# Performance work log

Measured on AMD Instinct MI355X. Metric: run time of the kernel, lower is better.

## Reference

```python
import jax, jax.numpy as jnp
import numpy as np

HIDDEN = 2048
HEADS = 16
HEAD_DIM = HIDDEN // HEADS


def setup_inputs() -> dict:
    key = jax.random.key(0)
    ks = jax.random.split(key, 9)
    s = 0.02
    return {
        "hidden_state": jax.random.normal(ks[0], (2, 2048, HIDDEN), dtype=jnp.float32),
        "Wq": jax.random.normal(ks[1], (HIDDEN, HIDDEN), dtype=jnp.float32) * s,
        "bq": jnp.zeros((HIDDEN,), dtype=jnp.float32),
        "Wk": jax.random.normal(ks[2], (HIDDEN, HIDDEN), dtype=jnp.float32) * s,
        "bk": jnp.zeros((HIDDEN,), dtype=jnp.float32),
        "Wv": jax.random.normal(ks[3], (HIDDEN, HIDDEN), dtype=jnp.float32) * s,
        "bv": jnp.zeros((HIDDEN,), dtype=jnp.float32),
        "Wo": jax.random.normal(ks[4], (HIDDEN, HIDDEN), dtype=jnp.float32) * s,
        "bo": jnp.zeros((HIDDEN,), dtype=jnp.float32),
    }


def _split_head(x):
    b, s, _ = x.shape
    return x.reshape(b, s, HEADS, HEAD_DIM).transpose(0, 2, 1, 3)  # [B,H,S,D]


def reference(hidden_state, Wq, bq, Wk, bk, Wv, bv, Wo, bo):
    scale = 1.0 / (HEAD_DIM ** 0.5)
    # nn.Linear: x @ W.T + b
    q = _split_head(hidden_state @ Wq.T + bq)
    k = _split_head(hidden_state @ Wk.T + bk)
    v = _split_head(hidden_state @ Wv.T + bv)
    scores = jnp.einsum("bhqd,bhkd->bhqk", q, k) * scale  # [B,H,S,S]
    probs = jax.nn.softmax(scores, axis=-1)
    # dropout treated as identity (eval mode)
    out = jnp.einsum("bhqk,bhkd->bhqd", probs, v)  # [B,H,S,D]
    b, h, s, d = out.shape
    out = out.transpose(0, 2, 1, 3).reshape(b, s, h * d)
    return out @ Wo.T + bo
```

## Files before the change

kernel.cpp:

```cpp
#include <hip/hip_runtime.h>
#include <hip/hip_bf16.h>


typedef __attribute__((ext_vector_type(8))) short bf16x8;
typedef __attribute__((ext_vector_type(4))) float f32x4;
typedef unsigned short ushort_t;

#define MFMA_16x16x32(a, b, c) __builtin_amdgcn_mfma_f32_16x16x32_bf16((a), (b), (c), 0, 0, 0)

__device__ __forceinline__ ushort_t f2bf(float f) {
  unsigned int u = __builtin_bit_cast(unsigned int, f);
  u += 0x7fffu + ((u >> 16) & 1u);
  return (ushort_t)(u >> 16);
}

__device__ __forceinline__ void gload_lds16(const void* g, void* lds) {
  __builtin_amdgcn_global_load_lds(
      (const __attribute__((address_space(1))) unsigned int*)g,
      (__attribute__((address_space(3))) unsigned int*)(unsigned int)(unsigned long long)lds,
      16, 0, 0);
}

__global__ __launch_bounds__(256) void f2bf_kernel(const float* __restrict__ in,
                                                   ushort_t* __restrict__ out, int n4) {
  int i = blockIdx.x * blockDim.x + threadIdx.x;
  const int stride = gridDim.x * blockDim.x;
  for (; i < n4; i += stride) {
    const float4 v = ((const float4*)in)[i];
    ushort4 o;
    o.x = f2bf(v.x); o.y = f2bf(v.y); o.z = f2bf(v.z); o.w = f2bf(v.w);
    ((ushort4*)out)[i] = o;
  }
}

template <int SWAPV>
__global__ __launch_bounds__(512) void qkv_gemm(
    const ushort_t* __restrict__ A,
    const ushort_t* __restrict__ W,
    const float* __restrict__ bq, const float* __restrict__ bk,
    const float* __restrict__ bv,
    ushort_t* __restrict__ Qs, ushort_t* __restrict__ Ks,
    ushort_t* __restrict__ Vts, int nbx, int bcol0) {
  constexpr int K = 2048, NT = K / 32;
  extern __shared__ char sm[];
  const int tid = threadIdx.x;
  const int wave = tid >> 6, lane = tid & 63;
  const int g = lane >> 4, l15 = lane & 15;
  const int wr = wave >> 2, wc = wave & 3;

  const int bid = blockIdx.x;
  const int chunk = (nbx * 16) >> 3;
  const int sw = (bid & 7) * chunk + (bid >> 3);
  const int bx = sw % nbx, by = sw / nbx;
  const int brow = by * 256, bcol = bcol0 + bx * 256;

  const ushort_t* srcA[2];
  const ushort_t* srcB[2];
#pragma unroll
  for (int j = 0; j < 2; ++j) {
    const int p = (wave * 2 + j) * 64 + lane;
    const int row = p >> 2;
    const int col = (p & 3) ^ ((row >> 1) & 3);
    srcA[j] = A + (size_t)(brow + row) * K + col * 8;
    srcB[j] = W + (size_t)(bcol + row) * K + col * 8;
  }

  const int fph = (l15 >> 1) & 3;
  const int aOff = (wr * 128 + l15) * 64 + ((g ^ fph) << 4);
  const int bOff = (wc * 64 + l15) * 64 + ((g ^ fph) << 4) + 16384;

  char* p0 = sm;
  char* p1 = sm + 32768;
  char* p2 = sm + 65536;

#define STAGE_A(P, t)                                                        \
  {                                                                          \
    gload_lds16(srcA[0] + (t) * 32, (P) + (wave * 2 + 0) * 1024);            \
    gload_lds16(srcA[1] + (t) * 32, (P) + (wave * 2 + 1) * 1024);            \
  }
#define STAGE_B(P, t)                                                        \
  {                                                                          \
    gload_lds16(srcB[0] + (t) * 32, (P) + 16384 + (wave * 2 + 0) * 1024);    \
    gload_lds16(srcB[1] + (t) * 32, (P) + 16384 + (wave * 2 + 1) * 1024);    \
  }

  const f32x4 fzero = {0.f, 0.f, 0.f, 0.f};
  f32x4 acc[8][4];
#pragma unroll
  for (int i = 0; i < 8; ++i)
#pragma unroll
    for (int j = 0; j < 4; ++j) acc[i][j] = fzero;

  STAGE_A(p0, 0); STAGE_B(p0, 0);
  STAGE_A(p1, 1); STAGE_B(p1, 1);
  asm volatile("s_waitcnt vmcnt(4)" ::: "memory");
  __builtin_amdgcn_sched_barrier(0);
  __builtin_amdgcn_s_barrier();
  __builtin_amdgcn_sched_barrier(0);

  for (int kt = 0; kt < NT; ++kt) {
    const bool doStage = (kt < NT - 2);
    if (doStage) STAGE_A(p2, kt + 2);
    bf16x8 bfr[4], afr[4];
#pragma unroll
    for (int j = 0; j < 4; ++j) bfr[j] = *(const bf16x8*)(p0 + bOff + j * 1024);
#pragma unroll
    for (int i = 0; i < 4; ++i) afr[i] = *(const bf16x8*)(p0 + aOff + i * 1024);
    __builtin_amdgcn_s_setprio(1);
#pragma unroll
    for (int i = 0; i < 4; ++i)
#pragma unroll
      for (int j = 0; j < 4; ++j)
        acc[i][j] = SWAPV ? MFMA_16x16x32(bfr[j], afr[i], acc[i][j])
                          : MFMA_16x16x32(afr[i], bfr[j], acc[i][j]);
    __builtin_amdgcn_s_setprio(0);
    if (doStage) STAGE_B(p2, kt + 2);
#pragma unroll
    for (int i = 0; i < 4; ++i) afr[i] = *(const bf16x8*)(p0 + aOff + (4 + i) * 1024);
    __builtin_amdgcn_s_setprio(1);
#pragma unroll
    for (int i = 0; i < 4; ++i)
#pragma unroll
      for (int j = 0; j < 4; ++j)
        acc[4 + i][j] = SWAPV ? MFMA_16x16x32(bfr[j], afr[i], acc[4 + i][j])
                              : MFMA_16x16x32(afr[i], bfr[j], acc[4 + i][j]);
    __builtin_amdgcn_s_setprio(0);
    if (doStage) {
      asm volatile("s_waitcnt vmcnt(4) lgkmcnt(0)" ::: "memory");
    } else {
      asm volatile("s_waitcnt vmcnt(0) lgkmcnt(0)" ::: "memory");
    }
    __builtin_amdgcn_sched_barrier(0);
    __builtin_amdgcn_s_barrier();
    __builtin_amdgcn_sched_barrier(0);
    char* t = p0; p0 = p1; p1 = p2; p2 = t;
  }
#undef STAGE_A
#undef STAGE_B

  if (!SWAPV) {
    const int seg = bcol >> 11;
    const float* bias = (seg == 0) ? bq : bk;
    ushort_t* out = (seg == 0) ? Qs : Ks;
#pragma unroll
    for (int j = 0; j < 4; ++j) {
      const int n = (bcol + wc * 64 + j * 16 + l15) & 2047;
      const float bb = bias[n];
      const int h = n >> 7, d = n & 127;
#pragma unroll
      for (int i = 0; i < 8; ++i) {
#pragma unroll
        for (int r = 0; r < 4; ++r) {
          const int grow = brow + wr * 128 + i * 16 + g * 4 + r;
          const int b_ = grow >> 11, s_ = grow & 2047;
          out[(((size_t)b_ * 16 + h) * 2048 + s_) * 128 + d] =
              f2bf(acc[i][j][r] + bb);
        }
      }
    }
  } else {
#pragma unroll
    for (int j = 0; j < 4; ++j) {
#pragma unroll
      for (int r = 0; r < 4; ++r) {
        const int n = (bcol + wc * 64 + j * 16 + g * 4 + r) & 2047;
        const float bb = bv[n];
        const int h = n >> 7, d = n & 127;
#pragma unroll
        for (int i = 0; i < 8; ++i) {
          const int m = brow + wr * 128 + i * 16 + l15;
          const int b_ = m >> 11, s_ = m & 2047;
          Vts[(((size_t)b_ * 16 + h) * 128 + d) * 2048 + s_] =
              f2bf(acc[i][j][r] + bb);
        }
      }
    }
  }
}

__global__ __launch_bounds__(256) void gemm_bt_kernel(const ushort_t* __restrict__ A,
                                                      const ushort_t* __restrict__ B,
                                                      const float* __restrict__ bias,
                                                      float* __restrict__ Cout,
                                                      int M, int N, int K) {
  __shared__ __align__(16) char smem[16384];
  char* sA = smem;
  char* sB = smem + 8192;
  const int tid = threadIdx.x;
  const int wave = tid >> 6;
  const int lane = tid & 63;
  const int wr = wave >> 1, wc = wave & 1;
  const int brow = blockIdx.y * 128;
  const int bcol = blockIdx.x * 128;

  const f32x4 fzero = {0.f, 0.f, 0.f, 0.f};
  f32x4 acc[4][4];
#pragma unroll
  for (int i = 0; i < 4; ++i)
#pragma unroll
    for (int j = 0; j < 4; ++j) acc[i][j] = fzero;

  const int srow = lane >> 2;
  const int koff = (lane & 3) * 8;

  for (int kt = 0; kt < K; kt += 32) {
#pragma unroll
    for (int c = 0; c < 2; ++c) {
      const int ch = wave + c * 4;
      gload_lds16(A + (size_t)(brow + ch * 16 + srow) * K + kt + koff, sA + ch * 1024);
      gload_lds16(B + (size_t)(bcol + ch * 16 + srow) * K + kt + koff, sB + ch * 1024);
    }
    __syncthreads();
    bf16x8 af[4], bfr[4];
#pragma unroll
    for (int i = 0; i < 4; ++i)
      af[i] = *(const bf16x8*)(sA + (wr * 64 + i * 16 + (lane & 15)) * 64 + (lane >> 4) * 16);
#pragma unroll
    for (int j = 0; j < 4; ++j)
      bfr[j] = *(const bf16x8*)(sB + (wc * 64 + j * 16 + (lane & 15)) * 64 + (lane >> 4) * 16);
#pragma unroll
    for (int i = 0; i < 4; ++i)
#pragma unroll
      for (int j = 0; j < 4; ++j) acc[i][j] = MFMA_16x16x32(af[i], bfr[j], acc[i][j]);
    __syncthreads();
  }

#pragma unroll
  for (int i = 0; i < 4; ++i)
#pragma unroll
    for (int j = 0; j < 4; ++j)
#pragma unroll
      for (int r = 0; r < 4; ++r) {
        const int row = brow + wr * 64 + i * 16 + (lane >> 4) * 4 + r;
        const int col = bcol + wc * 64 + j * 16 + (lane & 15);
        Cout[(size_t)row * N + col] = acc[i][j][r] + bias[col];
      }
}

__global__ __launch_bounds__(256) void attn_kernel(const ushort_t* __restrict__ Q,
                                                   const ushort_t* __restrict__ K,
                                                   const ushort_t* __restrict__ Vt,
                                                   ushort_t* __restrict__ O) {
  constexpr int S = 2048, D = 128, H = 16;
  __shared__ __align__(16) char smem[16384 + 16384 + 9216];
  char* sK = smem;
  char* sVt = smem + 16384;
  char* sP = smem + 32768;

  const int tid = threadIdx.x;
  const int wave = tid >> 6;
  const int lane = tid & 63;
  const int g = lane >> 4;
  const int l15 = lane & 15;
  const int qt = blockIdx.x & 31;
  const int bh = blockIdx.x >> 5;
  const int b = bh >> 4, h = bh & 15;

  const ushort_t* Qb = Q + (size_t)bh * S * D;
  const char* Kb = (const char*)(K + (size_t)bh * S * D);
  const char* Vtb = (const char*)(Vt + (size_t)bh * D * S);
  const int q0 = qt * 64 + wave * 16;

  bf16x8 aq[4];
  {
    const ushort_t* qrow = Qb + (size_t)(q0 + l15) * D + g * 8;
#pragma unroll
    for (int kk = 0; kk < 4; ++kk) aq[kk] = *(const bf16x8*)(qrow + kk * 32);
  }

  const char* kg[4];
  const char* vg[4];
#pragma unroll
  for (int i = 0; i < 4; ++i) {
    const int po = (wave * 4 + i) * 1024 + lane * 16;
    const int lk = po ^ (((po >> 8) & 7) << 4);
    kg[i] = Kb + (size_t)(lk >> 8) * 256 + (lk & 255);
    const int lv = po ^ (((po >> 7) & 7) << 4);
    vg[i] = Vtb + (size_t)(lv >> 7) * 4096 + (lv & 127);
  }

  const f32x4 fzero = {0.f, 0.f, 0.f, 0.f};
  f32x4 o[8];
#pragma unroll
  for (int nt = 0; nt < 8; ++nt) o[nt] = fzero;
  float row_m[4] = {-1e30f, -1e30f, -1e30f, -1e30f};
  float row_l[4] = {0.f, 0.f, 0.f, 0.f};

  char* sPw = sP + wave * 2304;
  const float scale = 0.08838834764831845f;
  const float LOG2E = 1.4426950408889634f;

  for (int kv0 = 0; kv0 < S; kv0 += 64) {
    __syncthreads();
#pragma unroll
    for (int i = 0; i < 4; ++i)
      gload_lds16(kg[i] + (size_t)kv0 * 256, sK + (wave * 4 + i) * 1024);
#pragma unroll
    for (int i = 0; i < 4; ++i)
      gload_lds16(vg[i] + (size_t)kv0 * 2, sVt + (wave * 4 + i) * 1024);
    __syncthreads();

    f32x4 sfrag[4];
#pragma unroll
    for (int nt = 0; nt < 4; ++nt) {
      sfrag[nt] = fzero;
#pragma unroll
      for (int kk = 0; kk < 4; ++kk) {
        const int row = nt * 16 + l15;
        const int la = row * 256 + kk * 64 + g * 16;
        const bf16x8 bk = *(const bf16x8*)(sK + (la ^ ((row & 7) << 4)));
        sfrag[nt] = MFMA_16x16x32(aq[kk], bk, sfrag[nt]);
      }
    }

#pragma unroll
    for (int r = 0; r < 4; ++r) {
      const float s0 = sfrag[0][r] * scale;
      const float s1 = sfrag[1][r] * scale;
      const float s2 = sfrag[2][r] * scale;
      const float s3 = sfrag[3][r] * scale;
      float mx = fmaxf(fmaxf(s0, s1), fmaxf(s2, s3));
      mx = fmaxf(mx, __shfl_xor(mx, 1));
      mx = fmaxf(mx, __shfl_xor(mx, 2));
      mx = fmaxf(mx, __shfl_xor(mx, 4));
      mx = fmaxf(mx, __shfl_xor(mx, 8));
      if (!__all(mx - row_m[r] <= 8.0f)) {
        const float nm = fmaxf(row_m[r], mx);
        const float corr = exp2f((row_m[r] - nm) * LOG2E);
        row_l[r] *= corr;
#pragma unroll
        for (int nt = 0; nt < 8; ++nt) o[nt][r] *= corr;
        row_m[r] = nm;
      }
      const float nm = row_m[r];
      const float p0 = exp2f((s0 - nm) * LOG2E);
      const float p1 = exp2f((s1 - nm) * LOG2E);
      const float p2 = exp2f((s2 - nm) * LOG2E);
      const float p3 = exp2f((s3 - nm) * LOG2E);
      float rs = (p0 + p1) + (p2 + p3);
      rs += __shfl_xor(rs, 1);
      rs += __shfl_xor(rs, 2);
      rs += __shfl_xor(rs, 4);
      rs += __shfl_xor(rs, 8);
      row_l[r] += rs;
      ushort_t* pr = (ushort_t*)(sPw + (g * 4 + r) * 144);
      pr[l15] = f2bf(p0);
      pr[16 + l15] = f2bf(p1);
      pr[32 + l15] = f2bf(p2);
      pr[48 + l15] = f2bf(p3);
    }

    const bf16x8 pa0 = *(const bf16x8*)(sPw + l15 * 144 + g * 16);
    const bf16x8 pa1 = *(const bf16x8*)(sPw + l15 * 144 + 64 + g * 16);
#pragma unroll
    for (int nt = 0; nt < 8; ++nt) {
      const int d = nt * 16 + l15;
      const int la0 = d * 128 + g * 16;
      const bf16x8 bv0 = *(const bf16x8*)(sVt + (la0 ^ ((d & 7) << 4)));
      o[nt] = MFMA_16x16x32(pa0, bv0, o[nt]);
      const bf16x8 bv1 = *(const bf16x8*)(sVt + ((la0 + 64) ^ ((d & 7) << 4)));
      o[nt] = MFMA_16x16x32(pa1, bv1, o[nt]);
    }
  }

#pragma unroll
  for (int r = 0; r < 4; ++r) {
    const float inv = 1.0f / row_l[r];
    const int srow = q0 + g * 4 + r;
    ushort_t* orow = O + ((size_t)b * S + srow) * (H * D) + h * D;
#pragma unroll
    for (int nt = 0; nt < 8; ++nt) orow[nt * 16 + l15] = f2bf(o[nt][r] * inv);
  }
}

extern "C" void kernel_launch(void* const* d_in, const int* in_sizes, int n_in,
                              void* d_out, int out_size, void* d_ws, size_t ws_size,
                              hipStream_t stream) {
  const float* hidden = (const float*)d_in[0];
  const float* Wq = (const float*)d_in[1];
  const float* bq = (const float*)d_in[2];
  const float* Wk = (const float*)d_in[3];
  const float* bk = (const float*)d_in[4];
  const float* Wv = (const float*)d_in[5];
  const float* bv = (const float*)d_in[6];
  const float* Wo = (const float*)d_in[7];
  const float* bo = (const float*)d_in[8];

  constexpr int M = 4096, N = 2048, Kd = 2048;
  char* ws = (char*)d_ws;
  ushort_t* hb   = (ushort_t*)(ws);
  ushort_t* wqkv = (ushort_t*)(ws + (16u << 20));
  ushort_t* wob  = (ushort_t*)(ws + (40u << 20));
  ushort_t* Qs   = (ushort_t*)(ws + (48u << 20));
  ushort_t* Ks   = Qs + (size_t)M * N;
  ushort_t* Vts  = Ks + (size_t)M * N;
  ushort_t* AO   = Vts + (size_t)M * N;

  f2bf_kernel<<<2048, 256, 0, stream>>>(hidden, hb, M * Kd / 4);
  f2bf_kernel<<<1024, 256, 0, stream>>>(Wq, wqkv, N * Kd / 4);
  f2bf_kernel<<<1024, 256, 0, stream>>>(Wk, wqkv + (size_t)N * Kd, N * Kd / 4);
  f2bf_kernel<<<1024, 256, 0, stream>>>(Wv, wqkv + 2 * (size_t)N * Kd, N * Kd / 4);
  f2bf_kernel<<<1024, 256, 0, stream>>>(Wo, wob, N * Kd / 4);

  qkv_gemm<0><<<256, 512, 98304, stream>>>(hb, wqkv, bq, bk, bv, Qs, Ks, Vts, 16, 0);
  qkv_gemm<1><<<128, 512, 98304, stream>>>(hb, wqkv, bq, bk, bv, Qs, Ks, Vts, 8, 4096);
  attn_kernel<<<1024, 256, 0, stream>>>(Qs, Ks, Vts, AO);
  dim3 gg(N / 128, M / 128);
  gemm_bt_kernel<<<gg, 256, 0, stream>>>(AO, wob, bo, (float*)d_out, M, N, Kd);
}
```

Before: 538.3 us.

## Cut softmax shuffles: lazy max reduction, MFMA row sums, packed bf16 convert

```diff
diff --git a/kernel.cpp b/kernel.cpp
--- a/kernel.cpp
+++ b/kernel.cpp
@@ -286,9 +286,13 @@
   float row_m[4] = {-1e30f, -1e30f, -1e30f, -1e30f};
   float row_l[4] = {0.f, 0.f, 0.f, 0.f};
 
+  bf16x8 ones;
+#pragma unroll
+  for (int i = 0; i < 8; ++i) ones[i] = (short)0x3F80;
+
   char* sPw = sP + wave * 2304;
-  const float scale = 0.08838834764831845f;
-  const float LOG2E = 1.4426950408889634f;
+  const float SC = 0.12751746f;
+  const float THR = 90.0f;
 
   for (int kv0 = 0; kv0 < S; kv0 += 64) {
     __syncthreads();
@@ -315,43 +319,44 @@
 
 #pragma unroll
     for (int r = 0; r < 4; ++r) {
-      const float s0 = sfrag[0][r] * scale;
-      const float s1 = sfrag[1][r] * scale;
-      const float s2 = sfrag[2][r] * scale;
-      const float s3 = sfrag[3][r] * scale;
-      float mx = fmaxf(fmaxf(s0, s1), fmaxf(s2, s3));
-      mx = fmaxf(mx, __shfl_xor(mx, 1));
-      mx = fmaxf(mx, __shfl_xor(mx, 2));
-      mx = fmaxf(mx, __shfl_xor(mx, 4));
-      mx = fmaxf(mx, __shfl_xor(mx, 8));
-      if (!__all(mx - row_m[r] <= 8.0f)) {
+      const float s0 = sfrag[0][r];
+      const float s1 = sfrag[1][r];
+      const float s2 = sfrag[2][r];
+      const float s3 = sfrag[3][r];
+      const float lm = fmaxf(fmaxf(s0, s1), fmaxf(s2, s3));
+      if (!__all(lm - row_m[r] <= THR)) {
+        float mx = lm;
+        mx = fmaxf(mx, __shfl_xor(mx, 1));
+        mx = fmaxf(mx, __shfl_xor(mx, 2));
+        mx = fmaxf(mx, __shfl_xor(mx, 4));
+        mx = fmaxf(mx, __shfl_xor(mx, 8));
         const float nm = fmaxf(row_m[r], mx);
-        const float corr = exp2f((row_m[r] - nm) * LOG2E);
+        const float corr = exp2f((row_m[r] - nm) * SC);
         row_l[r] *= corr;
 #pragma unroll
         for (int nt = 0; nt < 8; ++nt) o[nt][r] *= corr;
         row_m[r] = nm;
       }
       const float nm = row_m[r];
-      const float p0 = exp2f((s0 - nm) * LOG2E);
-      const float p1 = exp2f((s1 - nm) * LOG2E);
-      const float p2 = exp2f((s2 - nm) * LOG2E);
-      const float p3 = exp2f((s3 - nm) * LOG2E);
-      float rs = (p0 + p1) + (p2 + p3);
-      rs += __shfl_xor(rs, 1);
-      rs += __shfl_xor(rs, 2);
-      rs += __shfl_xor(rs, 4);
-      rs += __shfl_xor(rs, 8);
-      row_l[r] += rs;
+      const float p0 = exp2f((s0 - nm) * SC);
+      const float p1 = exp2f((s1 - nm) * SC);
+      const float p2 = exp2f((s2 - nm) * SC);
+      const float p3 = exp2f((s3 - nm) * SC);
+      unsigned int pk01, pk23;
+      asm("v_cvt_pk_bf16_f32 %0, %1, %2" : "=v"(pk01) : "v"(p0), "v"(p1));
+      asm("v_cvt_pk_bf16_f32 %0, %1, %2" : "=v"(pk23) : "v"(p2), "v"(p3));
       ushort_t* pr = (ushort_t*)(sPw + (g * 4 + r) * 144);
-      pr[l15] = f2bf(p0);
-      pr[16 + l15] = f2bf(p1);
-      pr[32 + l15] = f2bf(p2);
-      pr[48 + l15] = f2bf(p3);
+      pr[l15] = (ushort_t)(pk01 & 0xffffu);
+      pr[16 + l15] = (ushort_t)(pk01 >> 16);
+      pr[32 + l15] = (ushort_t)(pk23 & 0xffffu);
+      pr[48 + l15] = (ushort_t)(pk23 >> 16);
     }
 
     const bf16x8 pa0 = *(const bf16x8*)(sPw + l15 * 144 + g * 16);
     const bf16x8 pa1 = *(const bf16x8*)(sPw + l15 * 144 + 64 + g * 16);
+    f32x4 lfrag = fzero;
+    lfrag = MFMA_16x16x32(pa0, ones, lfrag);
+    lfrag = MFMA_16x16x32(pa1, ones, lfrag);
 #pragma unroll
     for (int nt = 0; nt < 8; ++nt) {
       const int d = nt * 16 + l15;
@@ -361,6 +366,8 @@
       const bf16x8 bv1 = *(const bf16x8*)(sVt + ((la0 + 64) ^ ((d & 7) << 4)));
       o[nt] = MFMA_16x16x32(pa1, bv1, o[nt]);
     }
+#pragma unroll
+    for (int r = 0; r < 4; ++r) row_l[r] += lfrag[r];
   }
 
 #pragma unroll
```

Result: faster. 489.5 us (-9.1%).
